# Kernel optimization log

Measured on AMD Instinct MI355X. Metric: run time of the kernel, lower is better.

## Reference

```python
import jax, jax.numpy as jnp
import numpy as np

# Complete 32-ary tree of depth 3: vocab = 32**3 = 32768 leaves.
B = 4096       # batch
NHID = 512     # hidden size
BR = 32        # branching factor (num_children at every internal node)
DEPTH = 3      # number of internal-node decisions from root to leaf
V = BR ** DEPTH
NUM_NODES = sum(BR ** k for k in range(DEPTH))  # 1 + 32 + 1024 = 1057

# Static tree-indexing tables (level-order node numbering).
_LEVEL_OFFSET = np.array([sum(BR ** j for j in range(k)) for k in range(DEPTH)], dtype=np.int64)   # [0, 1, 33]
_NODE_DIV = np.array([BR ** (DEPTH - k) for k in range(DEPTH)], dtype=np.int64)                    # node-within-level divisor
_STEP_DIV = np.array([BR ** (DEPTH - 1 - k) for k in range(DEPTH)], dtype=np.int64)                # child-step divisor


def setup_inputs() -> dict:
    key = jax.random.key(0)
    k1, k2, k3 = jax.random.split(key, 3)
    inputs = jax.random.normal(k1, (B, NHID), dtype=jnp.float32)
    labels = jax.random.randint(k2, (B,), 0, V)                     # leaf index per sample
    W = jax.random.normal(k3, (NUM_NODES, NHID, BR), dtype=jnp.float32)  # all node params, stacked
    return {"inputs": inputs, "labels": labels, "W": W}


def reference(inputs, labels, W):
    lab = labels[:, None]                                            # [B, 1]
    node_idx = jnp.asarray(_LEVEL_OFFSET)[None, :] + lab // jnp.asarray(_NODE_DIV)[None, :]  # [B, D] node on path
    steps = (lab // jnp.asarray(_STEP_DIV)[None, :]) % BR            # [B, D] child taken at each node
    Wg = W[node_idx]                                                 # [B, D, NHID, BR] gathered path params
    logits = jnp.einsum('bh,bdhc->bdc', inputs, Wg)                  # [B, D, BR]
    p = jax.nn.softmax(logits, axis=-1)
    step_p = jnp.take_along_axis(p, steps[:, :, None], axis=-1)[..., 0]  # [B, D]
    return jnp.prod(step_p, axis=-1)                                 # [B] path probability
```

## Files before the change

kernel.cpp:

```cpp
#include <hip/hip_runtime.h>


#define B_SZ 4096
#define NHID 512
#define BR 32
#define DEPTH 3

__global__ __launch_bounds__(192) void hsm_kernel(
    const float* __restrict__ inputs,
    const int* __restrict__ labels,
    const float* __restrict__ W,
    float* __restrict__ out)
{
    __shared__ float xs[NHID];
    __shared__ float pk[DEPTH];

    const int b = blockIdx.x;
    const int tid = threadIdx.x;

    if (tid < NHID / 4) {
        ((float4*)xs)[tid] = ((const float4*)(inputs + (size_t)b * NHID))[tid];
    }
    __syncthreads();

    const int k    = tid >> 6;
    const int lane = tid & 63;
    const int lab  = labels[b];

    int node, step;
    if (k == 0)      { node = 0;                 step = (lab >> 10) & 31; }
    else if (k == 1) { node = 1 + (lab >> 10);   step = (lab >> 5)  & 31; }
    else             { node = 33 + (lab >> 5);   step = lab & 31;         }

    const int colg  = lane & 7;
    const int hbase = lane >> 3;
    const float4* wp = (const float4*)(W + (size_t)node * (NHID * BR) + hbase * BR + colg * 4);

    float a0 = 0.f, a1 = 0.f, a2 = 0.f, a3 = 0.f;
    #pragma unroll 8
    for (int i = 0; i < NHID / 8; ++i) {
        float4 w = wp[i * (8 * BR / 4)];
        float  x = xs[hbase + 8 * i];
        a0 = fmaf(x, w.x, a0);
        a1 = fmaf(x, w.y, a1);
        a2 = fmaf(x, w.z, a2);
        a3 = fmaf(x, w.w, a3);
    }

    for (int m = 8; m <= 32; m <<= 1) {
        a0 += __shfl_xor(a0, m);
        a1 += __shfl_xor(a1, m);
        a2 += __shfl_xor(a2, m);
        a3 += __shfl_xor(a3, m);
    }

    float mx = fmaxf(fmaxf(a0, a1), fmaxf(a2, a3));
    for (int m = 1; m <= 4; m <<= 1) mx = fmaxf(mx, __shfl_xor(mx, m));
    float es = expf(a0 - mx) + expf(a1 - mx) + expf(a2 - mx) + expf(a3 - mx);
    for (int m = 1; m <= 4; m <<= 1) es += __shfl_xor(es, m);

    const int e = step & 3;
    float v = (e == 0) ? a0 : (e == 1) ? a1 : (e == 2) ? a2 : a3;
    float sl = __shfl(v, step >> 2);

    float p = __expf(sl - mx) / es;
    p = expf(sl - mx) / es;

    if (lane == 0) pk[k] = p;
    __syncthreads();
    if (tid == 0) out[b] = pk[0] * pk[1] * pk[2];
}

extern "C" void kernel_launch(void* const* d_in, const int* in_sizes, int n_in,
                              void* d_out, int out_size, void* d_ws, size_t ws_size,
                              hipStream_t stream)
{
    const float* inputs = (const float*)d_in[0];
    const int*   labels = (const int*)d_in[1];
    const float* W      = (const float*)d_in[2];
    float* out = (float*)d_out;

    hsm_kernel<<<dim3(B_SZ), dim3(192), 0, stream>>>(inputs, labels, W, out);
}
```

Measured before the change: 134.9 us.

## Bucket samples by level-2 node and process each bucket in one block

Adds a histogram, scan and scatter pass that groups batch rows by their deepest internal node (label>>5). Each compute block then handles every sample of one bucket, one sample per wavefront, so that node's weights are reused through cache across those samples. The goal is to cut repeated global traffic for W gathers. The cost is three extra small kernels plus a memset. The compute grid shrinks to 1024 blocks of uneven size, and the weight-reuse loop is still per-sample, so it only gains through cache hits.

```diff
diff --git a/kernel.cpp b/kernel.cpp
--- a/kernel.cpp
+++ b/kernel.cpp
@@ -1,74 +1,118 @@
 #include <hip/hip_runtime.h>
 
 
-#define B_SZ 4096
-#define NHID 512
-#define BR 32
-#define DEPTH 3
+#define NHID   512
+#define BR     32
+#define BATCH  4096
+#define NBUCK  1024
+#define CHUNK  8
 
-__global__ __launch_bounds__(192) void hsm_kernel(
+
+__global__ void k_hist(const int* __restrict__ labels, int* __restrict__ counts) {
+    int t = blockIdx.x * blockDim.x + threadIdx.x;
+    if (t < BATCH) atomicAdd(&counts[labels[t] >> 5], 1);
+}
+
+__global__ __launch_bounds__(1024) void k_scan(const int* __restrict__ counts,
+                                               int* __restrict__ offs) {
+    __shared__ int tmp[NBUCK];
+    int t = threadIdx.x;
+    tmp[t] = counts[t];
+    __syncthreads();
+    for (int d = 1; d < NBUCK; d <<= 1) {
+        int v = (t >= d) ? tmp[t - d] : 0;
+        __syncthreads();
+        tmp[t] += v;
+        __syncthreads();
+    }
+    offs[t] = tmp[t] - counts[t];
+}
+
+__global__ void k_scatter(const int* __restrict__ labels, const int* __restrict__ offs,
+                          int* __restrict__ cursor, int* __restrict__ order) {
+    int t = blockIdx.x * blockDim.x + threadIdx.x;
+    if (t < BATCH) {
+        int g = labels[t] >> 5;
+        int pos = offs[g] + atomicAdd(&cursor[g], 1);
+        order[pos] = t;
+    }
+}
+
+__global__ __launch_bounds__(256) void k_compute(
     const float* __restrict__ inputs,
     const int* __restrict__ labels,
     const float* __restrict__ W,
+    const int* __restrict__ counts,
+    const int* __restrict__ offs,
+    const int* __restrict__ order,
     float* __restrict__ out)
 {
-    __shared__ float xs[NHID];
-    __shared__ float pk[DEPTH];
+    __shared__ float xs[CHUNK][NHID];
 
-    const int b = blockIdx.x;
-    const int tid = threadIdx.x;
+    const int g = blockIdx.x;
+    const int n = counts[g];
+    if (n == 0) return;
+    const int base0 = offs[g];
 
-    if (tid < NHID / 4) {
-        ((float4*)xs)[tid] = ((const float4*)(inputs + (size_t)b * NHID))[tid];
-    }
-    __syncthreads();
-
-    const int k    = tid >> 6;
+    const int tid  = threadIdx.x;
+    const int wave = tid >> 6;
     const int lane = tid & 63;
-    const int lab  = labels[b];
-
-    int node, step;
-    if (k == 0)      { node = 0;                 step = (lab >> 10) & 31; }
-    else if (k == 1) { node = 1 + (lab >> 10);   step = (lab >> 5)  & 31; }
-    else             { node = 33 + (lab >> 5);   step = lab & 31;         }
-
     const int colg  = lane & 7;
     const int hbase = lane >> 3;
-    const float4* wp = (const float4*)(W + (size_t)node * (NHID * BR) + hbase * BR + colg * 4);
 
-    float a0 = 0.f, a1 = 0.f, a2 = 0.f, a3 = 0.f;
-    #pragma unroll 8
-    for (int i = 0; i < NHID / 8; ++i) {
-        float4 w = wp[i * (8 * BR / 4)];
-        float  x = xs[hbase + 8 * i];
-        a0 = fmaf(x, w.x, a0);
-        a1 = fmaf(x, w.y, a1);
-        a2 = fmaf(x, w.z, a2);
-        a3 = fmaf(x, w.w, a3);
+    for (int base = 0; base < n; base += CHUNK) {
+        const int m = min(CHUNK, n - base);
+        __syncthreads();
+        for (int idx = tid; idx < m * (NHID / 4); idx += 256) {
+            int r = idx >> 7;
+            int c = idx & 127;
+            int id = order[base0 + base + r];
+            ((float4*)xs[r])[c] = ((const float4*)(inputs + (size_t)id * NHID))[c];
+        }
+        __syncthreads();
+
+        for (int s = wave; s < m; s += 4) {
+            const int id  = order[base0 + base + s];
+            const int lab = labels[id];
+            float p = 1.0f;
+            #pragma unroll
+            for (int k = 0; k < 3; ++k) {
+                int node, step;
+                if (k == 0)      { node = 0;                 step = (lab >> 10) & 31; }
+                else if (k == 1) { node = 1 + (lab >> 10);   step = (lab >> 5)  & 31; }
+                else             { node = 33 + (lab >> 5);   step = lab & 31;         }
+
+                const float4* wp = (const float4*)(W + (size_t)node * (NHID * BR))
+                                   + hbase * (BR / 4) + colg;
+                float a0 = 0.f, a1 = 0.f, a2 = 0.f, a3 = 0.f;
+                #pragma unroll 8
+                for (int i = 0; i < NHID / 8; ++i) {
+                    float4 w = wp[i * (8 * BR / 4)];
+                    float  x = xs[s][hbase + 8 * i];
+                    a0 = fmaf(x, w.x, a0);
+                    a1 = fmaf(x, w.y, a1);
+                    a2 = fmaf(x, w.z, a2);
+                    a3 = fmaf(x, w.w, a3);
+                }
+                for (int mm = 8; mm <= 32; mm <<= 1) {
+                    a0 += __shfl_xor(a0, mm);
+                    a1 += __shfl_xor(a1, mm);
+                    a2 += __shfl_xor(a2, mm);
+                    a3 += __shfl_xor(a3, mm);
+                }
+                float mx = fmaxf(fmaxf(a0, a1), fmaxf(a2, a3));
+                for (int mm = 1; mm <= 4; mm <<= 1) mx = fmaxf(mx, __shfl_xor(mx, mm));
+                float es = expf(a0 - mx) + expf(a1 - mx) + expf(a2 - mx) + expf(a3 - mx);
+                for (int mm = 1; mm <= 4; mm <<= 1) es += __shfl_xor(es, mm);
+
+                int e = step & 3;
+                float v = (e == 0) ? a0 : (e == 1) ? a1 : (e == 2) ? a2 : a3;
+                float sl = __shfl(v, step >> 2);
+                p *= expf(sl - mx) / es;
+            }
+            if (lane == 0) out[id] = p;
+        }
     }
-
-    for (int m = 8; m <= 32; m <<= 1) {
-        a0 += __shfl_xor(a0, m);
-        a1 += __shfl_xor(a1, m);
-        a2 += __shfl_xor(a2, m);
-        a3 += __shfl_xor(a3, m);
-    }
-
-    float mx = fmaxf(fmaxf(a0, a1), fmaxf(a2, a3));
-    for (int m = 1; m <= 4; m <<= 1) mx = fmaxf(mx, __shfl_xor(mx, m));
-    float es = expf(a0 - mx) + expf(a1 - mx) + expf(a2 - mx) + expf(a3 - mx);
-    for (int m = 1; m <= 4; m <<= 1) es += __shfl_xor(es, m);
-
-    const int e = step & 3;
-    float v = (e == 0) ? a0 : (e == 1) ? a1 : (e == 2) ? a2 : a3;
-    float sl = __shfl(v, step >> 2);
-
-    float p = __expf(sl - mx) / es;
-    p = expf(sl - mx) / es;
-
-    if (lane == 0) pk[k] = p;
-    __syncthreads();
-    if (tid == 0) out[b] = pk[0] * pk[1] * pk[2];
 }
 
 extern "C" void kernel_launch(void* const* d_in, const int* in_sizes, int n_in,
@@ -80,5 +124,16 @@
     const float* W      = (const float*)d_in[2];
     float* out = (float*)d_out;
 
-    hsm_kernel<<<dim3(B_SZ), dim3(192), 0, stream>>>(inputs, labels, W, out);
+    char* ws = (char*)d_ws;
+    int* counts = (int*)(ws);
+    int* offs   = (int*)(ws + 4096);
+    int* cursor = (int*)(ws + 8192);
+    int* order  = (int*)(ws + 12288);
+
+    hipMemsetAsync(ws, 0, 12288, stream);
+    k_hist   <<<dim3(BATCH / 256), dim3(256), 0, stream>>>(labels, counts);
+    k_scan   <<<dim3(1),           dim3(NBUCK), 0, stream>>>(counts, offs);
+    k_scatter<<<dim3(BATCH / 256), dim3(256), 0, stream>>>(labels, offs, cursor, order);
+    k_compute<<<dim3(NBUCK),       dim3(256), 0, stream>>>(inputs, labels, W,
+                                                           counts, offs, order, out);
 }
```

After: 151.0 us. +11.9%, slower.

## Bucket samples by leaf-parent node to reuse weights across samples in one block

Applied to the files above, without the earlier changes.

Launches one block per level-2 node; each block scans all labels to collect the samples routed through its node, then computes logits for up to eight samples at a time against the shared root, level-1 and level-2 weight matrices. This amortizes weight loads across samples instead of reloading every path node per sample, and uses DPP cross-lane adds for partial reductions. It adds a redundant full-label scan per block and a fixed per-bucket capacity, beyond which samples would be dropped.

```diff
diff --git a/kernel.cpp b/kernel.cpp
--- a/kernel.cpp
+++ b/kernel.cpp
@@ -1,74 +1,158 @@
 #include <hip/hip_runtime.h>
 
 
-#define B_SZ 4096
-#define NHID 512
-#define BR 32
-#define DEPTH 3
+#define NHID  512
+#define BR    32
+#define BATCH 4096
+#define NBUCK 1024
+#define SMAX  8
+#define SCAP  64
 
-__global__ __launch_bounds__(192) void hsm_kernel(
+__device__ __forceinline__ float dpp_xadd1(float v) {
+    int m = __builtin_amdgcn_update_dpp(0, __float_as_int(v), 0xB1, 0xF, 0xF, true);
+    return v + __int_as_float(m);
+}
+__device__ __forceinline__ float dpp_xadd2(float v) {
+    int m = __builtin_amdgcn_update_dpp(0, __float_as_int(v), 0x4E, 0xF, 0xF, true);
+    return v + __int_as_float(m);
+}
+
+#define FMA4(A, xv, wv_) do { \
+    (A).x = fmaf((xv), (wv_).x, (A).x); \
+    (A).y = fmaf((xv), (wv_).y, (A).y); \
+    (A).z = fmaf((xv), (wv_).z, (A).z); \
+    (A).w = fmaf((xv), (wv_).w, (A).w); } while (0)
+
+__global__ __launch_bounds__(256, 4) void hsm_fused(
     const float* __restrict__ inputs,
     const int* __restrict__ labels,
     const float* __restrict__ W,
     float* __restrict__ out)
 {
-    __shared__ float xs[NHID];
-    __shared__ float pk[DEPTH];
+    __shared__ float xsT[NHID * SMAX];
+    __shared__ float partial[8 * SMAX * 8 * 4];
+    __shared__ float pk[3][SMAX];
+    __shared__ int   slist[SCAP];
+    __shared__ int   scount;
 
-    const int b = blockIdx.x;
+    const int g   = blockIdx.x;
     const int tid = threadIdx.x;
 
-    if (tid < NHID / 4) {
-        ((float4*)xs)[tid] = ((const float4*)(inputs + (size_t)b * NHID))[tid];
+    if (tid == 0) scount = 0;
+    __syncthreads();
+
+    #pragma unroll
+    for (int r = 0; r < BATCH / 256; ++r) {
+        int j = tid + 256 * r;
+        int lab = labels[j];
+        if ((lab >> 5) == g) {
+            int p = atomicAdd(&scount, 1);
+            if (p < SCAP) slist[p] = (j << 5) | (lab & 31);
+        }
     }
     __syncthreads();
+    const int n = min(scount, SCAP);
+    if (n == 0) return;
 
-    const int k    = tid >> 6;
+    const int wv   = tid >> 6;
     const int lane = tid & 63;
-    const int lab  = labels[b];
+    const int hsel = lane & 7;
+    const int colg = lane >> 3;
 
-    int node, step;
-    if (k == 0)      { node = 0;                 step = (lab >> 10) & 31; }
-    else if (k == 1) { node = 1 + (lab >> 10);   step = (lab >> 5)  & 31; }
-    else             { node = 33 + (lab >> 5);   step = lab & 31;         }
+    const int node1 = 1 + (g >> 5);
+    const int node2 = 33 + g;
 
-    const int colg  = lane & 7;
-    const int hbase = lane >> 3;
-    const float4* wp = (const float4*)(W + (size_t)node * (NHID * BR) + hbase * BR + colg * 4);
+    for (int c0 = 0; c0 < n; c0 += SMAX) {
+        const int m = min(SMAX, n - c0);
 
-    float a0 = 0.f, a1 = 0.f, a2 = 0.f, a3 = 0.f;
-    #pragma unroll 8
-    for (int i = 0; i < NHID / 8; ++i) {
-        float4 w = wp[i * (8 * BR / 4)];
-        float  x = xs[hbase + 8 * i];
-        a0 = fmaf(x, w.x, a0);
-        a1 = fmaf(x, w.y, a1);
-        a2 = fmaf(x, w.z, a2);
-        a3 = fmaf(x, w.w, a3);
+        __syncthreads();
+        #pragma unroll
+        for (int r = 0; r < 2; ++r) {
+            int h = tid + 256 * r;
+            float vals[SMAX];
+            #pragma unroll
+            for (int s = 0; s < SMAX; ++s) {
+                float v = 0.0f;
+                if (s < m) {
+                    int sid = slist[c0 + s] >> 5;
+                    v = inputs[(size_t)sid * NHID + h];
+                }
+                vals[s] = v;
+            }
+            float4* dst = (float4*)&xsT[h * SMAX];
+            dst[0] = make_float4(vals[0], vals[1], vals[2], vals[3]);
+            dst[1] = make_float4(vals[4], vals[5], vals[6], vals[7]);
+        }
+        __syncthreads();
+
+        #pragma unroll
+        for (int k = 0; k < 3; ++k) {
+            const int node = (k == 0) ? 0 : (k == 1) ? node1 : node2;
+
+            const float4* wp = (const float4*)(W + (size_t)node * (NHID * BR))
+                               + wv * 1024 + hsel * 8 + colg;
+            const float4* xp = (const float4*)xsT + (128 * wv + hsel) * 2;
+
+            float4 acc[SMAX];
+            #pragma unroll
+            for (int s = 0; s < SMAX; ++s) acc[s] = make_float4(0, 0, 0, 0);
+
+            #pragma unroll 4
+            for (int i = 0; i < 16; ++i) {
+                float4 w4 = wp[i * 64];
+                float4 xa = xp[i * 16];
+                float4 xb = xp[i * 16 + 1];
+                FMA4(acc[0], xa.x, w4); FMA4(acc[1], xa.y, w4);
+                FMA4(acc[2], xa.z, w4); FMA4(acc[3], xa.w, w4);
+                FMA4(acc[4], xb.x, w4); FMA4(acc[5], xb.y, w4);
+                FMA4(acc[6], xb.z, w4); FMA4(acc[7], xb.w, w4);
+            }
+
+            #pragma unroll
+            for (int s = 0; s < SMAX; ++s) {
+                acc[s].x = dpp_xadd2(dpp_xadd1(acc[s].x));
+                acc[s].y = dpp_xadd2(dpp_xadd1(acc[s].y));
+                acc[s].z = dpp_xadd2(dpp_xadd1(acc[s].z));
+                acc[s].w = dpp_xadd2(dpp_xadd1(acc[s].w));
+            }
+            if ((lane & 3) == 0) {
+                int wq = wv * 2 + ((lane >> 2) & 1);
+                #pragma unroll
+                for (int s = 0; s < SMAX; ++s)
+                    *(float4*)&partial[((wq * SMAX + s) * 8 + colg) * 4] = acc[s];
+            }
+            __syncthreads();
+
+            {
+                int s   = tid >> 5;
+                int col = tid & 31;
+                int cg  = col >> 2, cc = col & 3;
+                float l = 0.0f;
+                #pragma unroll
+                for (int wq = 0; wq < 8; ++wq)
+                    l += partial[((wq * SMAX + s) * 8 + cg) * 4 + cc];
+                float mx = l;
+                #pragma unroll
+                for (int mm = 1; mm <= 16; mm <<= 1)
+                    mx = fmaxf(mx, __shfl_xor(mx, mm));
+                float e = expf(l - mx);
+                float es = e;
+                #pragma unroll
+                for (int mm = 1; mm <= 16; mm <<= 1)
+                    es += __shfl_xor(es, mm);
+                int step = (k == 0) ? (g >> 5)
+                         : (k == 1) ? (g & 31)
+                                    : (slist[c0 + s] & 31);
+                if (col == step) pk[k][s] = e / es;
+            }
+            __syncthreads();
+        }
+
+        if (tid < m) {
+            int sid = slist[c0 + tid] >> 5;
+            out[sid] = pk[0][tid] * pk[1][tid] * pk[2][tid];
+        }
     }
-
-    for (int m = 8; m <= 32; m <<= 1) {
-        a0 += __shfl_xor(a0, m);
-        a1 += __shfl_xor(a1, m);
-        a2 += __shfl_xor(a2, m);
-        a3 += __shfl_xor(a3, m);
-    }
-
-    float mx = fmaxf(fmaxf(a0, a1), fmaxf(a2, a3));
-    for (int m = 1; m <= 4; m <<= 1) mx = fmaxf(mx, __shfl_xor(mx, m));
-    float es = expf(a0 - mx) + expf(a1 - mx) + expf(a2 - mx) + expf(a3 - mx);
-    for (int m = 1; m <= 4; m <<= 1) es += __shfl_xor(es, m);
-
-    const int e = step & 3;
-    float v = (e == 0) ? a0 : (e == 1) ? a1 : (e == 2) ? a2 : a3;
-    float sl = __shfl(v, step >> 2);
-
-    float p = __expf(sl - mx) / es;
-    p = expf(sl - mx) / es;
-
-    if (lane == 0) pk[k] = p;
-    __syncthreads();
-    if (tid == 0) out[b] = pk[0] * pk[1] * pk[2];
 }
 
 extern "C" void kernel_launch(void* const* d_in, const int* in_sizes, int n_in,
@@ -80,5 +164,5 @@
     const float* W      = (const float*)d_in[2];
     float* out = (float*)d_out;
 
-    hsm_kernel<<<dim3(B_SZ), dim3(192), 0, stream>>>(inputs, labels, W, out);
+    hsm_fused<<<dim3(NBUCK), dim3(256), 0, stream>>>(inputs, labels, W, out);
 }
```

Result: faster. 126.8 us (-6.0%).

## Bucket-sort samples by leaf parent node and remap blocks for XCD locality

Applied to the files above, without the earlier changes.

Adds a single-block counting-sort kernel that orders batch samples by their level-2 node (label>>5), then has each main-kernel block take its sample from this order. The block index is remapped so consecutive sorted samples land on the same XCD (round-robin over 8), which is meant to raise L2 reuse of the 64KB per-node weight slices shared by samples with the same node. It adds an extra kernel launch and a serial single-block sort, plus an indirection load per block.

```diff
diff --git a/kernel.cpp b/kernel.cpp
--- a/kernel.cpp
+++ b/kernel.cpp
@@ -1,21 +1,61 @@
 #include <hip/hip_runtime.h>
 
 
-#define B_SZ 4096
-#define NHID 512
-#define BR 32
-#define DEPTH 3
+#define NHID  512
+#define BR    32
+#define BATCH 4096
+#define NBUCK 1024
+
+__global__ __launch_bounds__(1024) void k_sort(const int* __restrict__ labels,
+                                               int* __restrict__ order) {
+    __shared__ int labs[BATCH];
+    __shared__ int hist[NBUCK];
+    __shared__ int scn[NBUCK];
+    const int t = threadIdx.x;
+
+    hist[t] = 0;
+    #pragma unroll
+    for (int r = 0; r < BATCH / 1024; ++r)
+        labs[t + 1024 * r] = labels[t + 1024 * r];
+    __syncthreads();
+    #pragma unroll
+    for (int r = 0; r < BATCH / 1024; ++r)
+        atomicAdd(&hist[labs[t + 1024 * r] >> 5], 1);
+    __syncthreads();
+
+    const int cnt = hist[t];
+    scn[t] = cnt;
+    __syncthreads();
+    for (int d = 1; d < NBUCK; d <<= 1) {
+        int u = (t >= d) ? scn[t - d] : 0;
+        __syncthreads();
+        scn[t] += u;
+        __syncthreads();
+    }
+    hist[t] = scn[t] - cnt;
+    __syncthreads();
+
+    #pragma unroll
+    for (int r = 0; r < BATCH / 1024; ++r) {
+        int j = t + 1024 * r;
+        int pos = atomicAdd(&hist[labs[j] >> 5], 1);
+        order[pos] = j;
+    }
+}
 
 __global__ __launch_bounds__(192) void hsm_kernel(
     const float* __restrict__ inputs,
     const int* __restrict__ labels,
     const float* __restrict__ W,
+    const int* __restrict__ order,
     float* __restrict__ out)
 {
     __shared__ float xs[NHID];
-    __shared__ float pk[DEPTH];
+    __shared__ float pk[3];
 
-    const int b = blockIdx.x;
+    const int bidx = blockIdx.x;
+    const int r  = (bidx & 7) * (BATCH / 8) + (bidx >> 3);
+    const int b  = order[r];
     const int tid = threadIdx.x;
 
     if (tid < NHID / 4) {
@@ -62,9 +102,7 @@
     const int e = step & 3;
     float v = (e == 0) ? a0 : (e == 1) ? a1 : (e == 2) ? a2 : a3;
     float sl = __shfl(v, step >> 2);
-
-    float p = __expf(sl - mx) / es;
-    p = expf(sl - mx) / es;
+    float p = expf(sl - mx) / es;
 
     if (lane == 0) pk[k] = p;
     __syncthreads();
@@ -79,6 +117,8 @@
     const int*   labels = (const int*)d_in[1];
     const float* W      = (const float*)d_in[2];
     float* out = (float*)d_out;
+    int* order = (int*)d_ws;
 
-    hsm_kernel<<<dim3(B_SZ), dim3(192), 0, stream>>>(inputs, labels, W, out);
+    k_sort    <<<dim3(1),     dim3(1024), 0, stream>>>(labels, order);
+    hsm_kernel<<<dim3(BATCH), dim3(192),  0, stream>>>(inputs, labels, W, order, out);
 }
```

Measured after the change: 132.4 us. No clear change (-1.9%).
